# Optimization experiments

Hardware: AMD Instinct MI355X
Metric: run time of the kernel (lower is better)

Reference implementation:

```python
import jax, jax.numpy as jnp
import numpy as np

NUM_HEAD = 8
KEY_DIM = 256   # total key dim
VALUE_DIM = 256 # total value dim
OUT_DIM = 256
B, Q, K = 128, 384, 384


def setup_inputs() -> dict:
    key = jax.random.key(0)
    ks = jax.random.split(key, 11)
    hk = KEY_DIM // NUM_HEAD   # per-head key dim = 32
    hv = VALUE_DIM // NUM_HEAD # per-head value dim = 32
    s = 0.02
    return {
        "q_data": jax.random.normal(ks[0], (B, Q, KEY_DIM), jnp.float32),
        "m_data": jax.random.normal(ks[1], (B, K, VALUE_DIM), jnp.float32),
        "bias": jax.random.normal(ks[2], (B, 1, Q, K), jnp.float32),
        "nonbatched_bias": jax.random.normal(ks[3], (NUM_HEAD, Q, K), jnp.float32),
        "q_weights": jax.random.normal(ks[4], (KEY_DIM, NUM_HEAD, hk), jnp.float32) * s,
        "k_weights": jax.random.normal(ks[5], (VALUE_DIM, NUM_HEAD, hk), jnp.float32) * s,
        "v_weights": jax.random.normal(ks[6], (VALUE_DIM, NUM_HEAD, hv), jnp.float32) * s,
        "o_weights": jax.random.normal(ks[7], (NUM_HEAD, hv, OUT_DIM), jnp.float32) * s,
        "o_bias": jax.random.normal(ks[8], (OUT_DIM,), jnp.float32) * s,
        "gating_w": jax.random.normal(ks[9], (KEY_DIM, NUM_HEAD, hv), jnp.float32) * s,
        "gating_b": jnp.ones((NUM_HEAD, hv), jnp.float32),
    }


def reference(q_data, m_data, bias, nonbatched_bias,
              q_weights, k_weights, v_weights, o_weights, o_bias,
              gating_w, gating_b):
    hk = q_weights.shape[-1]
    scale = hk ** (-0.5)
    q = jnp.einsum('bqa,ahc->bqhc', q_data, q_weights) * scale
    k = jnp.einsum('bka,ahc->bkhc', m_data, k_weights)
    v = jnp.einsum('bka,ahc->bkhc', m_data, v_weights)
    # logits: [b,h,q,k] with additive pair bias and per-head nonbatched bias
    logits = jnp.einsum('bqhc,bkhc->bhqk', q, k) + bias + nonbatched_bias[None]
    weights = jax.nn.softmax(logits, axis=-1)
    weighted_avg = jnp.einsum('bhqk,bkhc->bqhc', weights, v)
    gate = jax.nn.sigmoid(jnp.einsum('bqc,chv->bqhv', q_data, gating_w) + gating_b)
    weighted_avg = weighted_avg * gate
    return jnp.einsum('bqhc,hco->bqo', weighted_avg, o_weights) + o_bias
```

## Files before the change

### kernel.cpp

```cpp
#include <hip/hip_runtime.h>
#include <hip/hip_bf16.h>

#define DM 256
#define NB 128
#define SQ 384
#define SK 384

typedef __bf16 bf16x4 __attribute__((ext_vector_type(4)));
typedef __bf16 bf16x8 __attribute__((ext_vector_type(8)));
typedef float f32x4 __attribute__((ext_vector_type(4)));
typedef unsigned short u16;
typedef unsigned int u32;

union BF8 { bf16x8 v8; bf16x4 v4[2]; uint2 u2[2]; };

__device__ __forceinline__ u16 f2bf(float f) {
    union { float fv; u32 u; } v; v.fv = f;
    u32 r = v.u + 0x7FFFu + ((v.u >> 16) & 1u);
    return (u16)(r >> 16);
}
__device__ __forceinline__ float bf2f(u16 u) {
    union { u32 v; float f; } x; x.v = ((u32)u) << 16; return x.f;
}
__device__ __forceinline__ uint2 pack4(float a, float b, float c, float d) {
    uint2 r;
    r.x = (u32)f2bf(a) | ((u32)f2bf(b) << 16);
    r.y = (u32)f2bf(c) | ((u32)f2bf(d) << 16);
    return r;
}
__device__ __forceinline__ uint2 pack4c(f32x4 v) {
    bf16x4 t;
    t[0] = (__bf16)v[0]; t[1] = (__bf16)v[1];
    t[2] = (__bf16)v[2]; t[3] = (__bf16)v[3];
    union { bf16x4 b; uint2 u; } cv; cv.b = t; return cv.u;
}
__device__ __forceinline__ void glds16(const void* g, void* l) {
    __builtin_amdgcn_global_load_lds(
        (const __attribute__((address_space(1))) unsigned int*)g,
        (__attribute__((address_space(3))) unsigned int*)l, 16, 0, 0);
}

__global__ __launch_bounds__(256)
void prep_w(const float* __restrict__ q_w, const float* __restrict__ k_w,
            const float* __restrict__ v_w, const float* __restrict__ g_w,
            const float* __restrict__ o_w, u16* __restrict__ wt)
{
    __shared__ float t[64][65];
    const int mat = blockIdx.z;
    const float* src = mat == 0 ? q_w : mat == 1 ? k_w : mat == 2 ? v_w : mat == 3 ? g_w : o_w;
    const float scale = (mat == 0) ? (float)(0.17677669529663687 * 1.4426950408889634) : 1.0f;
    const int k0 = blockIdx.x * 64, n0 = blockIdx.y * 64;
    const int tid = threadIdx.x;
#pragma unroll
    for (int i = 0; i < 4; ++i) {
        int pos = tid + i * 256;
        int r = pos >> 4, c4 = (pos & 15) * 4;
        f32x4 v = *(const f32x4*)&src[(size_t)(k0 + r) * DM + n0 + c4];
        t[r][c4 + 0] = v[0]; t[r][c4 + 1] = v[1]; t[r][c4 + 2] = v[2]; t[r][c4 + 3] = v[3];
    }
    __syncthreads();
    const int nr = tid >> 2, kq = (tid & 3) * 16;
    u16* dst = wt + (size_t)mat * DM * DM + (size_t)(n0 + nr) * DM + k0 + kq;
#pragma unroll
    for (int j = 0; j < 16; j += 4) {
        uint2 p = pack4(t[kq + j][nr] * scale, t[kq + j + 1][nr] * scale,
                        t[kq + j + 2][nr] * scale, t[kq + j + 3][nr] * scale);
        *(uint2*)&dst[j] = p;
    }
}

__global__ __launch_bounds__(256)
void prep_nb(const float* __restrict__ nb, float* __restrict__ nb2)
{
    int i = (blockIdx.x * 256 + threadIdx.x) * 4;
    f32x4 v = *(const f32x4*)&nb[i];
    *(f32x4*)&nb2[i] = v * 1.4426950408889634f - 20.0f;
}

template<int MODE>
__global__ __launch_bounds__(256)
void proj_kernel(const float* __restrict__ Af, const u16* __restrict__ Abf,
                 const u16* __restrict__ Wt1, const u16* __restrict__ Wt2,
                 const float* __restrict__ gb, const float* __restrict__ ob,
                 u16* __restrict__ out1, u16* __restrict__ gate,
                 u16* __restrict__ vT, float* __restrict__ outf)
{
    __shared__ u16 Wlds[64 * 256];
    const int tid = threadIdx.x, lane = tid & 63, w = tid >> 6;
    const int lr = lane & 15, lg = lane >> 4;
    const int m0 = blockIdx.x * 64;

    BF8 af[8];
    if (MODE <= 1) {
        const float* arow = Af + (size_t)(m0 + w * 16 + lr) * DM + 4 * lg;
#pragma unroll
        for (int ks = 0; ks < 8; ++ks) {
            f32x4 v0 = *(const f32x4*)&arow[ks * 32];
            f32x4 v1 = *(const f32x4*)&arow[ks * 32 + 16];
            af[ks].u2[0] = pack4(v0[0], v0[1], v0[2], v0[3]);
            af[ks].u2[1] = pack4(v1[0], v1[1], v1[2], v1[3]);
        }
    } else {
        const u16* arow = Abf + (size_t)(m0 + w * 16 + lr) * DM + 4 * lg;
#pragma unroll
        for (int ks = 0; ks < 8; ++ks) {
            af[ks].u2[0] = *(const uint2*)&arow[ks * 32];
            af[ks].u2[1] = *(const uint2*)&arow[ks * 32 + 16];
        }
    }

    const int NSLAB = (MODE == 2) ? 4 : 8;
    for (int sl = 0; sl < NSLAB; ++sl) {
        const u16* Wsrc = (sl < 4) ? Wt1 : Wt2;
        const int n0 = (sl & 3) * 64;
        if (sl) __syncthreads();
#pragma unroll
        for (int i = 0; i < 8; ++i) {
            int pos = tid + i * 256;
            int nr = pos >> 5, c8 = (pos & 31) * 8;
            uint4 gv = *(const uint4*)&Wsrc[(size_t)(n0 + nr) * DM + c8];
            int within = c8 & 31;
            int pa2 = (c8 >> 5) * 64 + ((within >> 3) & 1) * 32 + (within >> 4) * 8;
            int sw = (nr & 7) << 4;
            char* rb_ = (char*)Wlds + nr * 512;
            *(uint2*)(rb_ + (pa2 ^ sw)) = make_uint2(gv.x, gv.y);
            *(uint2*)(rb_ + ((pa2 + 16) ^ sw)) = make_uint2(gv.z, gv.w);
        }
        __syncthreads();

        f32x4 acc[4];
#pragma unroll
        for (int nf = 0; nf < 4; ++nf) acc[nf] = (f32x4){0.f, 0.f, 0.f, 0.f};
#pragma unroll
        for (int ks = 0; ks < 8; ++ks) {
#pragma unroll
            for (int nf = 0; nf < 4; ++nf) {
                int row = nf * 16 + lr;
                bf16x8 bfr = *(const bf16x8*)((char*)Wlds + row * 512 +
                                              ((ks * 64 + lg * 16) ^ ((row & 7) << 4)));
                acc[nf] = __builtin_amdgcn_mfma_f32_16x16x32_bf16(af[ks].v8, bfr, acc[nf], 0, 0, 0);
            }
        }

#pragma unroll
        for (int nf = 0; nf < 4; ++nf) {
            int n = n0 + nf * 16 + lr;
            int gn = (sl & 3) * 64 + nf * 16 + lr;
            if (MODE == 0) {
                if (sl < 4) {
#pragma unroll
                    for (int r = 0; r < 4; ++r)
                        out1[(size_t)(m0 + w * 16 + 4 * lg + r) * DM + n] = f2bf(acc[nf][r]);
                } else {
                    float gbv = gb[gn];
#pragma unroll
                    for (int r = 0; r < 4; ++r)
                        gate[(size_t)(m0 + w * 16 + 4 * lg + r) * DM + gn] =
                            f2bf(1.f / (1.f + __expf(-(acc[nf][r] + gbv))));
                }
            } else if (MODE == 1) {
                if (sl < 4) {
                    int pn = (n & ~31) | (((n >> 2) & 3) << 3) | (((n >> 4) & 1) << 2) | (n & 3);
#pragma unroll
                    for (int r = 0; r < 4; ++r)
                        out1[(size_t)(m0 + w * 16 + 4 * lg + r) * DM + pn] = f2bf(acc[nf][r]);
                } else {
                    int bb = m0 / SQ;
                    int kkl = m0 - bb * SQ + w * 16 + 4 * lg;
                    int cc = kkl & 31;
                    int kkp = (kkl & ~31) | (((cc >> 2) & 3) << 3) | (((cc >> 4) & 1) << 2);
                    *(uint2*)&vT[(size_t)(bb * DM + gn) * SK + kkp] =
                        pack4(acc[nf][0], acc[nf][1], acc[nf][2], acc[nf][3]);
                }
            } else {
                float obv = ob[n];
#pragma unroll
                for (int r = 0; r < 4; ++r)
                    outf[(size_t)(m0 + w * 16 + 4 * lg + r) * DM + n] = acc[nf][r] + obv;
            }
        }
    }
}

__global__ __launch_bounds__(512, 1)
void attn_kernel(const u16* __restrict__ Qb, const u16* __restrict__ Kb,
                 const u16* __restrict__ vT, const u16* __restrict__ gateb,
                 const float* __restrict__ bias, const float* __restrict__ nb2,
                 u16* __restrict__ wavg)
{
    extern __shared__ char smem[];
    const int tid = threadIdx.x, lane = tid & 63, h = tid >> 6;
    const int lr = lane & 15, lg = lane >> 4;
    const int bid = blockIdx.x;
    const int qt = bid >> 7, b = bid & 127;
    const int q0 = qt * 64;
    const float LOG2E = 1.4426950408889634f;

    const int ci0 = (h * 2) * 64 + lane, ci1 = (h * 2 + 1) * 64 + lane;
    const int kr0 = ci0 >> 5, kj0 = (ci0 & 31) ^ (kr0 & 7);
    const int kr1 = ci1 >> 5, kj1 = (ci1 & 31) ^ (kr1 & 7);
    const u16* kg0 = Kb + ((size_t)b * SK + kr0) * DM + kj0 * 8;
    const u16* kg1 = Kb + ((size_t)b * SK + kr1) * DM + kj1 * 8;
    const int vr0 = ci0 >> 2, vj0 = (ci0 & 3) ^ ((vr0 >> 1) & 3);
    const int vr1 = ci1 >> 2, vj1 = (ci1 & 3) ^ ((vr1 >> 1) & 3);
    const u16* vg0 = vT + ((size_t)b * DM + vr0) * SK + vj0 * 8;
    const u16* vg1 = vT + ((size_t)b * DM + vr1) * SK + vj1 * 8;
    const int cib = h * 64 + lane;
    const int bq = cib >> 3, bj = (cib & 7) ^ (bq & 7);
    const float* bg = bias + ((size_t)b * SQ + q0 + bq) * SK + bj * 4;

    const int kd0 = (h * 2) * 1024, kd1 = (h * 2 + 1) * 1024;
    const int bd = 32768 + h * 1024;

    BF8 qf[4];
    {
        const u16* qp = Qb + (size_t)(b * SQ + q0 + lr) * DM + h * 32 + 4 * lg;
#pragma unroll
        for (int nf = 0; nf < 4; ++nf) {
            qf[nf].u2[0] = *(const uint2*)&qp[nf * 16 * DM];
            qf[nf].u2[1] = *(const uint2*)&qp[nf * 16 * DM + 16];
        }
    }

    f32x4 Oacc[2][4];
    float lsum[4];
#pragma unroll
    for (int nf = 0; nf < 4; ++nf) {
        lsum[nf] = 0.f;
        Oacc[0][nf] = (f32x4){0.f, 0.f, 0.f, 0.f};
        Oacc[1][nf] = (f32x4){0.f, 0.f, 0.f, 0.f};
    }

    const float* np = nb2 + ((size_t)h * SQ + q0) * SK + 4 * lg;

    auto stage = [&](char* buf) {
        glds16(kg0, buf + kd0); glds16(kg1, buf + kd1);
        glds16(vg0, buf + 16384 + kd0); glds16(vg1, buf + 16384 + kd1);
        glds16(bg, buf + bd);
        kg0 += 32 * DM; kg1 += 32 * DM; vg0 += 32; vg1 += 32; bg += 32;
    };

    stage(smem);
    stage(smem + 40960);
    asm volatile("s_waitcnt vmcnt(5)" ::: "memory");
    __builtin_amdgcn_s_barrier();

#pragma unroll 1
    for (int kb = 0; kb < 12; ++kb) {
        const int k0 = kb * 32;
        char* buf = smem + (kb % 3) * 40960;
        char* Kc = buf; char* Vc = buf + 16384; char* Bc = buf + 32768;

        f32x4 n4r[4][2];
#pragma unroll
        for (int nf = 0; nf < 4; ++nf)
#pragma unroll
            for (int rb = 0; rb < 2; ++rb)
                n4r[nf][rb] = *(const f32x4*)&np[(size_t)(nf * 16 + lr) * SK + k0 + rb * 16];
        __builtin_amdgcn_sched_barrier(0);

        if (kb < 10) stage(smem + ((kb + 2) % 3) * 40960);

        f32x4 st[4][2];
        __builtin_amdgcn_s_setprio(1);
#pragma unroll
        for (int nf = 0; nf < 4; ++nf)
#pragma unroll
            for (int rb = 0; rb < 2; ++rb) {
                bf16x8 kfr = *(const bf16x8*)(Kc + (rb * 16 + lr) * 512 +
                                              (((h * 4 + lg) ^ (lr & 7)) << 4));
                st[nf][rb] = __builtin_amdgcn_mfma_f32_16x16x32_bf16(
                    kfr, qf[nf].v8, (f32x4){0.f, 0.f, 0.f, 0.f}, 0, 0, 0);
            }
        __builtin_amdgcn_s_setprio(0);

        BF8 pvv[4];
#pragma unroll
        for (int nf = 0; nf < 4; ++nf)
#pragma unroll
            for (int rb = 0; rb < 2; ++rb) {
                f32x4 b4 = *(const f32x4*)(Bc + (nf * 16 + lr) * 128 +
                                           (((rb * 4 + lg) ^ (lr & 7)) << 4));
                f32x4 s = st[nf][rb] + b4 * LOG2E + n4r[nf][rb];
                f32x4 e;
                e[0] = __builtin_amdgcn_exp2f(s[0]);
                e[1] = __builtin_amdgcn_exp2f(s[1]);
                e[2] = __builtin_amdgcn_exp2f(s[2]);
                e[3] = __builtin_amdgcn_exp2f(s[3]);
                lsum[nf] += (e[0] + e[1]) + (e[2] + e[3]);
                pvv[nf].u2[rb] = pack4c(e);
            }

        __builtin_amdgcn_s_setprio(1);
#pragma unroll
        for (int cf = 0; cf < 2; ++cf) {
            int row = h * 32 + cf * 16 + lr;
            bf16x8 vfr = *(const bf16x8*)(Vc + row * 64 + ((lg ^ ((lr >> 1) & 3)) << 4));
#pragma unroll
            for (int nf = 0; nf < 4; ++nf)
                Oacc[cf][nf] = __builtin_amdgcn_mfma_f32_16x16x32_bf16(
                    vfr, pvv[nf].v8, Oacc[cf][nf], 0, 0, 0);
        }
        __builtin_amdgcn_s_setprio(0);

        if (kb < 10)      asm volatile("s_waitcnt vmcnt(5)" ::: "memory");
        else if (kb == 10) asm volatile("s_waitcnt vmcnt(0)" ::: "memory");
        if (kb < 11) __builtin_amdgcn_s_barrier();
    }

#pragma unroll
    for (int nf = 0; nf < 4; ++nf) {
        lsum[nf] += __shfl_xor(lsum[nf], 16, 64);
        lsum[nf] += __shfl_xor(lsum[nf], 32, 64);
    }

#pragma unroll
    for (int nf = 0; nf < 4; ++nf) {
        float rl = 1.0f / lsum[nf];
        size_t qrow = (size_t)(b * SQ + q0 + nf * 16 + lr);
#pragma unroll
        for (int cf = 0; cf < 2; ++cf) {
            size_t idx = qrow * DM + h * 32 + cf * 16 + 4 * lg;
            uint2 g2 = *(const uint2*)&gateb[idx];
            float g0 = bf2f((u16)(g2.x & 0xffff)), g1 = bf2f((u16)(g2.x >> 16));
            float g2f = bf2f((u16)(g2.y & 0xffff)), g3 = bf2f((u16)(g2.y >> 16));
            f32x4 o = Oacc[cf][nf];
            *(uint2*)&wavg[idx] = pack4(o[0] * rl * g0, o[1] * rl * g1,
                                        o[2] * rl * g2f, o[3] * rl * g3);
        }
    }
}

extern "C" void kernel_launch(void* const* d_in, const int* in_sizes, int n_in,
                              void* d_out, int out_size, void* d_ws, size_t ws_size,
                              hipStream_t stream) {
    const float* q_data = (const float*)d_in[0];
    const float* m_data = (const float*)d_in[1];
    const float* bias   = (const float*)d_in[2];
    const float* nbias  = (const float*)d_in[3];
    const float* q_w    = (const float*)d_in[4];
    const float* k_w    = (const float*)d_in[5];
    const float* v_w    = (const float*)d_in[6];
    const float* o_w    = (const float*)d_in[7];
    const float* o_b    = (const float*)d_in[8];
    const float* g_w    = (const float*)d_in[9];
    const float* g_b    = (const float*)d_in[10];
    float* out = (float*)d_out;

    const size_t MB = (size_t)NB * SQ * DM * 2;
    char* ws = (char*)d_ws;
    u16* qb    = (u16*)(ws);
    u16* kb    = (u16*)(ws + MB);
    u16* vTb   = (u16*)(ws + 2 * MB);
    u16* gateb = (u16*)(ws + 3 * MB);
    u16* wavg  = (u16*)(ws + 4 * MB);
    u16* wt    = (u16*)(ws + 5 * MB);
    float* nb2 = (float*)(ws + 5 * MB + 655360);
    u16* Wtq = wt, *Wtk = wt + 65536, *Wtv = wt + 2 * 65536,
       *Wtg = wt + 3 * 65536, *Wto = wt + 4 * 65536;

    prep_w<<<dim3(4, 4, 5), 256, 0, stream>>>(q_w, k_w, v_w, g_w, o_w, wt);
    prep_nb<<<1152, 256, 0, stream>>>(nbias, nb2);
    proj_kernel<0><<<768, 256, 0, stream>>>(q_data, nullptr, Wtq, Wtg, g_b, nullptr,
                                            qb, gateb, nullptr, nullptr);
    proj_kernel<1><<<768, 256, 0, stream>>>(m_data, nullptr, Wtk, Wtv, nullptr, nullptr,
                                            kb, nullptr, vTb, nullptr);

    const int ATTN_SMEM = 3 * 40960;
    hipFuncSetAttribute((const void*)attn_kernel,
                        hipFuncAttributeMaxDynamicSharedMemorySize, ATTN_SMEM);
    attn_kernel<<<768, 512, ATTN_SMEM, stream>>>(qb, kb, vTb, gateb, bias, nb2, wavg);

    proj_kernel<2><<<768, 256, 0, stream>>>(nullptr, wavg, Wto, nullptr, nullptr, o_b,
                                            nullptr, nullptr, nullptr, out);
}
```

Baseline: 284.8 us.

## Split attention block by head groups and switch to double-buffered staging

Each attention block now handles 4 heads instead of 8, so there are twice as many 256-thread blocks. The K/V staging covers only half the channels per block. Shared memory drops from a triple buffer to a double buffer of smaller tiles, with a full vmcnt(0) wait each iteration. The smaller per-block footprint should let more blocks share a CU and raise occupancy. In exchange, the bias tile is loaded twice (once per head group), and the shallower prefetch pipeline may leave more load latency exposed.

```diff
diff --git a/kernel.cpp b/kernel.cpp
--- a/kernel.cpp
+++ b/kernel.cpp
@@ -182,35 +182,37 @@
     }
 }
 
-__global__ __launch_bounds__(512, 1)
+__global__ __launch_bounds__(256, 1)
 void attn_kernel(const u16* __restrict__ Qb, const u16* __restrict__ Kb,
                  const u16* __restrict__ vT, const u16* __restrict__ gateb,
                  const float* __restrict__ bias, const float* __restrict__ nb2,
                  u16* __restrict__ wavg)
 {
     extern __shared__ char smem[];
-    const int tid = threadIdx.x, lane = tid & 63, h = tid >> 6;
+    const int tid = threadIdx.x, lane = tid & 63, hw = tid >> 6;
     const int lr = lane & 15, lg = lane >> 4;
     const int bid = blockIdx.x;
-    const int qt = bid >> 7, b = bid & 127;
+    const int pair = bid >> 1, hg = bid & 1;
+    const int qt = pair >> 7, b = pair & 127;
     const int q0 = qt * 64;
+    const int h = hg * 4 + hw;
     const float LOG2E = 1.4426950408889634f;
 
-    const int ci0 = (h * 2) * 64 + lane, ci1 = (h * 2 + 1) * 64 + lane;
-    const int kr0 = ci0 >> 5, kj0 = (ci0 & 31) ^ (kr0 & 7);
-    const int kr1 = ci1 >> 5, kj1 = (ci1 & 31) ^ (kr1 & 7);
-    const u16* kg0 = Kb + ((size_t)b * SK + kr0) * DM + kj0 * 8;
-    const u16* kg1 = Kb + ((size_t)b * SK + kr1) * DM + kj1 * 8;
-    const int vr0 = ci0 >> 2, vj0 = (ci0 & 3) ^ ((vr0 >> 1) & 3);
-    const int vr1 = ci1 >> 2, vj1 = (ci1 & 3) ^ ((vr1 >> 1) & 3);
-    const u16* vg0 = vT + ((size_t)b * DM + vr0) * SK + vj0 * 8;
-    const u16* vg1 = vT + ((size_t)b * DM + vr1) * SK + vj1 * 8;
-    const int cib = h * 64 + lane;
-    const int bq = cib >> 3, bj = (cib & 7) ^ (bq & 7);
-    const float* bg = bias + ((size_t)b * SQ + q0 + bq) * SK + bj * 4;
-
-    const int kd0 = (h * 2) * 1024, kd1 = (h * 2 + 1) * 1024;
-    const int bd = 32768 + h * 1024;
+    const int ciA = hw * 64 + lane, ciB = 256 + hw * 64 + lane;
+    const int krA = ciA >> 4, kjA = (ciA & 15) ^ (krA & 7);
+    const int krB = ciB >> 4, kjB = (ciB & 15) ^ (krB & 7);
+    const u16* kgA = Kb + ((size_t)b * SK + krA) * DM + hg * 128 + kjA * 8;
+    const u16* kgB = Kb + ((size_t)b * SK + krB) * DM + hg * 128 + kjB * 8;
+    const int vrA = ciA >> 2, vjA = (ciA & 3) ^ ((vrA >> 1) & 3);
+    const int vrB = ciB >> 2, vjB = (ciB & 3) ^ ((vrB >> 1) & 3);
+    const u16* vgA = vT + ((size_t)b * DM + hg * 128 + vrA) * SK + vjA * 8;
+    const u16* vgB = vT + ((size_t)b * DM + hg * 128 + vrB) * SK + vjB * 8;
+    const int bqA = ciA >> 3, bjA = (ciA & 7) ^ (bqA & 7);
+    const int bqB = ciB >> 3, bjB = (ciB & 7) ^ (bqB & 7);
+    const float* bgA = bias + ((size_t)b * SQ + q0 + bqA) * SK + bjA * 4;
+    const float* bgB = bias + ((size_t)b * SQ + q0 + bqB) * SK + bjB * 4;
+
+    const int dA = hw * 1024, dB = 4096 + hw * 1024;
 
     BF8 qf[4];
     {
@@ -234,22 +236,22 @@
     const float* np = nb2 + ((size_t)h * SQ + q0) * SK + 4 * lg;
 
     auto stage = [&](char* buf) {
-        glds16(kg0, buf + kd0); glds16(kg1, buf + kd1);
-        glds16(vg0, buf + 16384 + kd0); glds16(vg1, buf + 16384 + kd1);
-        glds16(bg, buf + bd);
-        kg0 += 32 * DM; kg1 += 32 * DM; vg0 += 32; vg1 += 32; bg += 32;
+        glds16(kgA, buf + dA); glds16(kgB, buf + dB);
+        glds16(vgA, buf + 8192 + dA); glds16(vgB, buf + 8192 + dB);
+        glds16(bgA, buf + 16384 + dA); glds16(bgB, buf + 16384 + dB);
+        kgA += 32 * DM; kgB += 32 * DM; vgA += 32; vgB += 32; bgA += 32; bgB += 32;
     };
 
     stage(smem);
-    stage(smem + 40960);
-    asm volatile("s_waitcnt vmcnt(5)" ::: "memory");
+    asm volatile("s_waitcnt vmcnt(0)" ::: "memory");
     __builtin_amdgcn_s_barrier();
 
+    int cur = 0;
 #pragma unroll 1
     for (int kb = 0; kb < 12; ++kb) {
         const int k0 = kb * 32;
-        char* buf = smem + (kb % 3) * 40960;
-        char* Kc = buf; char* Vc = buf + 16384; char* Bc = buf + 32768;
+        char* buf = smem + cur * 24576;
+        char* Kc = buf; char* Vc = buf + 8192; char* Bc = buf + 16384;
 
         f32x4 n4r[4][2];
 #pragma unroll
@@ -259,7 +261,7 @@
                 n4r[nf][rb] = *(const f32x4*)&np[(size_t)(nf * 16 + lr) * SK + k0 + rb * 16];
         __builtin_amdgcn_sched_barrier(0);
 
-        if (kb < 10) stage(smem + ((kb + 2) % 3) * 40960);
+        if (kb < 11) stage(smem + (cur ^ 1) * 24576);
 
         f32x4 st[4][2];
         __builtin_amdgcn_s_setprio(1);
@@ -267,8 +269,8 @@
         for (int nf = 0; nf < 4; ++nf)
 #pragma unroll
             for (int rb = 0; rb < 2; ++rb) {
-                bf16x8 kfr = *(const bf16x8*)(Kc + (rb * 16 + lr) * 512 +
-                                              (((h * 4 + lg) ^ (lr & 7)) << 4));
+                bf16x8 kfr = *(const bf16x8*)(Kc + (rb * 16 + lr) * 256 +
+                                              (((hw * 4 + lg) ^ (lr & 7)) << 4));
                 st[nf][rb] = __builtin_amdgcn_mfma_f32_16x16x32_bf16(
                     kfr, qf[nf].v8, (f32x4){0.f, 0.f, 0.f, 0.f}, 0, 0, 0);
             }
@@ -294,7 +296,7 @@
         __builtin_amdgcn_s_setprio(1);
 #pragma unroll
         for (int cf = 0; cf < 2; ++cf) {
-            int row = h * 32 + cf * 16 + lr;
+            int row = hw * 32 + cf * 16 + lr;
             bf16x8 vfr = *(const bf16x8*)(Vc + row * 64 + ((lg ^ ((lr >> 1) & 3)) << 4));
 #pragma unroll
             for (int nf = 0; nf < 4; ++nf)
@@ -303,9 +305,11 @@
         }
         __builtin_amdgcn_s_setprio(0);
 
-        if (kb < 10)      asm volatile("s_waitcnt vmcnt(5)" ::: "memory");
-        else if (kb == 10) asm volatile("s_waitcnt vmcnt(0)" ::: "memory");
-        if (kb < 11) __builtin_amdgcn_s_barrier();
+        if (kb < 11) {
+            asm volatile("s_waitcnt vmcnt(0)" ::: "memory");
+            __builtin_amdgcn_s_barrier();
+            cur ^= 1;
+        }
     }
 
 #pragma unroll
@@ -366,10 +370,10 @@
     proj_kernel<1><<<768, 256, 0, stream>>>(m_data, nullptr, Wtk, Wtv, nullptr, nullptr,
                                             kb, nullptr, vTb, nullptr);
 
-    const int ATTN_SMEM = 3 * 40960;
+    const int ATTN_SMEM = 2 * 24576;
     hipFuncSetAttribute((const void*)attn_kernel,
                         hipFuncAttributeMaxDynamicSharedMemorySize, ATTN_SMEM);
-    attn_kernel<<<768, 512, ATTN_SMEM, stream>>>(qb, kb, vTb, gateb, bias, nb2, wavg);
+    attn_kernel<<<1536, 256, ATTN_SMEM, stream>>>(qb, kb, vTb, gateb, bias, nb2, wavg);
 
     proj_kernel<2><<<768, 256, 0, stream>>>(nullptr, wavg, Wto, nullptr, nullptr, o_b,
                                             nullptr, nullptr, nullptr, out);
```

Result: faster. 272.3 us (-4.4%).
